# Kernel optimization log

Hardware: AMD Instinct MI355X
Metric: run time of the kernel (lower is better)

## Reference

```python
import jax, jax.numpy as jnp
import numpy as np

ALPHA = 0.5
TEMP = 0.1
TEMP2 = 0.05  # hardcoded in nt_xent_loss2
NUM_CLASSES = 10
EPS = 1e-12


def setup_inputs() -> dict:
    key = jax.random.key(0)
    k1, k2, k3 = jax.random.split(key, 3)
    B, D, C = 4096, 256, NUM_CLASSES
    cls_feats = jax.random.normal(k1, (B, D), dtype=jnp.float32)
    predicts = jax.random.normal(k2, (B, C), dtype=jnp.float32)
    targets = jax.random.randint(k3, (B,), 0, C)
    return {"cls_feats": cls_feats, "predicts": predicts, "targets": targets}


def _nt_xent_loss(feats, labels):
    B = feats.shape[0]
    eye = jnp.eye(B, dtype=bool)
    same = labels[:, None] == labels[None, :]
    mask = (same & ~eye).astype(feats.dtype)            # positives, no diagonal
    s = jnp.einsum('bd,cd->bc', feats, feats) / TEMP     # [B,B]
    s = jnp.where(eye, 0.0, s)                           # subtract diag_embed(diag)
    logits = s - jax.lax.stop_gradient(jnp.max(s, axis=1, keepdims=True))
    log_denom = jnp.log(jnp.sum(jnp.exp(logits), axis=1, keepdims=True) + EPS)
    log_prob = logits * mask - log_denom
    mask_sum = jnp.sum(mask, axis=1)
    mask_sum = jnp.where(mask_sum == 0, 1.0, mask_sum)
    pos_logits = jnp.sum(mask * log_prob, axis=1) / mask_sum
    return -jnp.mean(pos_logits)


def _nt_xent_loss2(feats, labels):
    B = feats.shape[0]
    eye = jnp.eye(B, dtype=bool)
    same = labels[:, None] == labels[None, :]
    mask = (same & ~eye).astype(feats.dtype)
    diff = ~same                                         # mask2 / different-label pairs
    S = (feats @ feats.T) / TEMP2                        # [B,B]
    val = jnp.where(diff, S, 0.0)                        # dot * different_label_mask

    # The torch loop body depends only on labels[i] -> compute once per class.
    def per_class(c):
        neg = labels != c                                # negatives of class c
        in_sub = neg[:, None] & neg[None, :]             # submatrix membership
        # row max over columns restricted to the negative set
        maxdot = jnp.max(jnp.where(neg[None, :], val, -jnp.inf), axis=1)  # [B]
        shifted = jnp.where(in_sub, val - maxdot[:, None], -jnp.inf)
        s_c = jnp.sum(jnp.exp(shifted))                  # exp_terms.sum()
        n_c = jnp.sum(jnp.where(in_sub, diff, False).astype(jnp.float32))
        return s_c, n_c

    sums, counts = jax.lax.map(jax.checkpoint(per_class), jnp.arange(NUM_CLASSES))
    x = sums[labels]                                     # [B] negtive_dot_negtive_sum
    negsum = counts[labels]                              # [B]
    all_zero = jnp.all(negsum == 0)
    x = jnp.where(all_zero, x, x / negsum)
    log_prob_row = -jnp.log(x + EPS)                     # constant across each row
    mask_sum = jnp.sum(mask, axis=1)
    mask_sum_safe = jnp.where(mask_sum == 0, 1.0, mask_sum)
    pos_logits = (mask_sum * log_prob_row) / mask_sum_safe
    return -jnp.mean(pos_logits)


def reference(cls_feats, predicts, targets):
    norm = jnp.maximum(jnp.linalg.norm(cls_feats, axis=-1, keepdims=True), EPS)
    feats = cls_feats / norm                             # F.normalize(dim=-1)
    logp = jax.nn.log_softmax(predicts, axis=-1)
    ce = -jnp.mean(jnp.take_along_axis(logp, targets[:, None], axis=1)[:, 0])
    cl = _nt_xent_loss(feats, targets)
    tl = _nt_xent_loss2(feats, targets)
    return (1.0 - ALPHA) * ce + ALPHA * cl + 0.5 * ALPHA * tl
```

## Files before the change

### kernel.cpp

```cpp
#include <hip/hip_runtime.h>
#include <math.h>

#define B 4096
#define D 256
#define NC 10
#define LSC 257

typedef __attribute__((ext_vector_type(8))) short bf16x8;
typedef __attribute__((ext_vector_type(4))) float f32x4;

__device__ __forceinline__ unsigned short f2bf(float x) {
    unsigned int u = __float_as_uint(x);
    u += 0x7FFFu + ((u >> 16) & 1u);
    return (unsigned short)(u >> 16);
}

__global__ void prep_kernel(const float* __restrict__ feats, const float* __restrict__ pred,
                            const int* __restrict__ tg, unsigned short* __restrict__ fN,
                            int* __restrict__ h, float* __restrict__ scal) {
    __shared__ int histL[16];
    const int t = threadIdx.x, w = t >> 6, l = t & 63;
    const int r0 = blockIdx.x * 64;
    if (t < 16) histL[t] = 0;
    __syncthreads();
    for (int i = 0; i < 16; i++) {
        int row = r0 + w * 16 + i;
        float4 v = ((const float4*)feats)[row * 64 + l];
        float ss = v.x * v.x + v.y * v.y + v.z * v.z + v.w * v.w;
#pragma unroll
        for (int o = 1; o < 64; o <<= 1) ss += __shfl_xor(ss, o);
        float inv = 1.0f / fmaxf(sqrtf(ss), 1e-12f);
        ushort4 ov;
        ov.x = f2bf(v.x * inv); ov.y = f2bf(v.y * inv);
        ov.z = f2bf(v.z * inv); ov.w = f2bf(v.w * inv);
        ((ushort4*)fN)[row * 64 + l] = ov;
        if (l == 0) atomicAdd(&histL[tg[row]], 1);
    }
    __syncthreads();
    if (t < NC && histL[t]) atomicAdd(&h[t], histL[t]);
    if (w == 0) {
        int row = r0 + l;
        const float* p = pred + row * NC;
        float m = p[0];
#pragma unroll
        for (int c = 1; c < NC; c++) m = fmaxf(m, p[c]);
        float s = 0.f;
#pragma unroll
        for (int c = 0; c < NC; c++) s += __expf(p[c] - m);
        float v = m + logf(s) - p[tg[row]];
#pragma unroll
        for (int o = 1; o < 64; o <<= 1) v += __shfl_xor(v, o);
        if (l == 0) atomicAdd(&scal[0], v);
    }
}

__global__ void scatter_kernel(const unsigned short* __restrict__ fN, const int* __restrict__ tg,
                               const int* __restrict__ h, int* __restrict__ ccnt,
                               unsigned short* __restrict__ fP, int* __restrict__ labelP,
                               int* __restrict__ origIdx) {
    __shared__ int cntL[16], baseL[16], cbL[16];
    __shared__ int clsL[64], rankL[64];
    const int t = threadIdx.x, w = t >> 6, l = t & 63;
    const int r0 = blockIdx.x * 64;
    if (t < 16) cntL[t] = 0;
    __syncthreads();
    if (l == 0) {
        for (int i = 0; i < 16; i++) {
            int idx = w * 16 + i;
            int c = tg[r0 + idx];
            clsL[idx] = c;
            rankL[idx] = atomicAdd(&cntL[c], 1);
        }
    }
    if (t == 0) {
        int r = 0;
        for (int c = 0; c < NC; c++) { cbL[c] = r; r += h[c]; }
    }
    __syncthreads();
    if (t < NC) baseL[t] = cbL[t] + atomicAdd(&ccnt[t], cntL[t]);
    __syncthreads();
    for (int i = 0; i < 16; i++) {
        int idx = w * 16 + i;
        int row = r0 + idx;
        int pos = baseL[clsL[idx]] + rankL[idx];
        if (l == 0) { labelP[pos] = clsL[idx]; origIdx[pos] = row; }
        ((ushort4*)fP)[pos * 64 + l] = ((const ushort4*)fN)[row * 64 + l];
    }
}

__launch_bounds__(256)
__global__ void gemm_kernel(const unsigned short* __restrict__ fA,
                            const unsigned short* __restrict__ fP,
                            const int* __restrict__ tg, const int* __restrict__ labelP,
                            const int* __restrict__ origIdx,
                            float* __restrict__ E1, float* __restrict__ P1,
                            float* __restrict__ E2G, int* __restrict__ M2K) {
    __shared__ float sc[64 * LSC];
    __shared__ int labS[256];
    __shared__ int origS[256];
    __shared__ float E2L[64 * 11];
    __shared__ int M2L[64 * 11];
    __shared__ float E1L[64], P1L[64];

    const int t = threadIdx.x;
    const int w = t >> 6, l = t & 63;
    const int row0 = blockIdx.x * 64;
    const int colB = blockIdx.y * 256;

    labS[t] = labelP[colB + t];
    origS[t] = origIdx[colB + t];
    for (int s = t; s < 64 * 11; s += 256) { E2L[s] = 0.f; M2L[s] = 0; }
    if (t < 64) { E1L[t] = 0.f; P1L[t] = 0.f; }

    const int qr = l >> 4;
    const int lm = l & 15;
    const unsigned short* pa = fA + (row0 + lm) * D + qr * 8;
    const unsigned short* pb = fP + (colB + w * 64 + lm) * D + qr * 8;

    f32x4 acc[4][4];
#pragma unroll
    for (int mb = 0; mb < 4; mb++)
#pragma unroll
        for (int nb = 0; nb < 4; nb++) acc[mb][nb] = (f32x4){0.f, 0.f, 0.f, 0.f};

#pragma unroll 2
    for (int ks = 0; ks < 8; ks++) {
        bf16x8 af[4], bfr[4];
#pragma unroll
        for (int mb = 0; mb < 4; mb++) af[mb] = *(const bf16x8*)(pa + mb * 16 * D + ks * 32);
#pragma unroll
        for (int nb = 0; nb < 4; nb++) bfr[nb] = *(const bf16x8*)(pb + nb * 16 * D + ks * 32);
#pragma unroll
        for (int mb = 0; mb < 4; mb++)
#pragma unroll
            for (int nb = 0; nb < 4; nb++)
                acc[mb][nb] = __builtin_amdgcn_mfma_f32_16x16x32_bf16(af[mb], bfr[nb],
                                                                      acc[mb][nb], 0, 0, 0);
    }

#pragma unroll
    for (int mb = 0; mb < 4; mb++)
#pragma unroll
        for (int nb = 0; nb < 4; nb++) {
            int col = w * 64 + nb * 16 + lm;
#pragma unroll
            for (int r = 0; r < 4; r++)
                sc[(mb * 16 + qr * 4 + r) * LSC + col] = acc[mb][nb][r];
        }
    __syncthreads();

    const int rowg = row0 + l;
    const int li = tg[rowg];
    float e1sum = 0.f, p1sum = 0.f;
    int seg = -1; float segE = 0.f; int segK = 0;
    const float* srow = sc + l * LSC + w * 64;
    for (int j = 0; j < 64; j++) {
        float g = srow[j];
        int cl = w * 64 + j;
        int lj = labS[cl];
        int oj = origS[cl];
        bool diag = (oj == rowg);
        bool same = (lj == li);
        float s1 = diag ? 0.f : 10.f * g;
        float e1 = __expf(s1);
        e1sum += e1;
        p1sum += (same && !diag) ? s1 : 0.f;
        if (lj != seg) {
            if (seg >= 0) {
                if (segE > 0.f) atomicAdd(&E2L[l * 11 + seg], segE);
                if (segK > 0) atomicMax(&M2L[l * 11 + seg], segK);
            }
            seg = lj; segE = 0.f; segK = 0;
        }
        if (!same) {
            segE += e1 * e1;
            segK = max(segK, __float_as_int(20.f * g + 64.f));
        }
    }
    if (seg >= 0) {
        if (segE > 0.f) atomicAdd(&E2L[l * 11 + seg], segE);
        if (segK > 0) atomicMax(&M2L[l * 11 + seg], segK);
    }
    atomicAdd(&E1L[l], e1sum);
    atomicAdd(&P1L[l], p1sum);
    __syncthreads();

    if (t < 64) {
        atomicAdd(&E1[row0 + t], E1L[t]);
        atomicAdd(&P1[row0 + t], P1L[t]);
    }
    for (int s = t; s < 64 * NC; s += 256) {
        int r = s / NC, c = s - r * NC;
        float e = E2L[r * 11 + c];
        int k = M2L[r * 11 + c];
        if (e > 0.f) atomicAdd(&E2G[(row0 + r) * NC + c], e);
        if (k > 0) atomicMax(&M2K[(row0 + r) * NC + c], k);
    }
}

__global__ void rowfin_kernel(const int* __restrict__ tg, const int* __restrict__ h,
                              const float* __restrict__ E1, const float* __restrict__ P1,
                              const float* __restrict__ E2G, const int* __restrict__ M2K,
                              float* __restrict__ sums, float* __restrict__ scal) {
    __shared__ float ssumL[16];
    const int t = threadIdx.x;
    if (t < 16) ssumL[t] = 0.f;
    __syncthreads();
    const int i = blockIdx.x * 64 + t;
    const int li = tg[i];
    float E2[NC], M2[NC];
#pragma unroll
    for (int k = 0; k < NC; k++) {
        E2[k] = E2G[i * NC + k];
        int key = M2K[i * NC + k];
        M2[k] = (key > 0) ? (__int_as_float(key) - 64.f) : -3.0e38f;
    }
    const int hl = h[li];
    E2[li] = (float)hl;
    M2[li] = 0.f;
    float m1 = -3.0e38f, m2 = -3.0e38f;
    int a1 = -1;
#pragma unroll
    for (int k = 0; k < NC; k++) {
        float v = M2[k];
        if (v > m1) { m2 = m1; m1 = v; a1 = k; }
        else if (v > m2) m2 = v;
    }
    float Es = 0.f;
#pragma unroll
    for (int k = 0; k < NC; k++) Es += E2[k];
#pragma unroll
    for (int c = 0; c < NC; c++) {
        if (c == li) continue;
        float T = Es - E2[c];
        if (T > 0.f) {
            float md = (a1 == c) ? m2 : m1;
            atomicAdd(&ssumL[c], __expf(-md) * T);
        }
    }
    float cn = (float)(hl - 1);
    float pos1 = (cn > 0.f) ? (P1[i] / cn - logf(E1[i])) : 0.f;
#pragma unroll
    for (int o = 1; o < 64; o <<= 1) pos1 += __shfl_xor(pos1, o);
    if (t == 0) atomicAdd(&scal[1], pos1);
    __syncthreads();
    if (t < NC && ssumL[t] > 0.f) atomicAdd(&sums[t], ssumL[t]);
}

__global__ void final_kernel(const int* __restrict__ h, const float* __restrict__ sums,
                             const float* __restrict__ scal, float* __restrict__ out) {
    if (threadIdx.x != 0) return;
    int hh[NC];
    long long S2 = 0;
    for (int c = 0; c < NC; c++) { hh[c] = h[c]; S2 += (long long)hh[c] * hh[c]; }
    float ncs[NC];
    int az = 1;
    for (int c = 0; c < NC; c++) {
        long long M = (long long)B - hh[c];
        long long n = M * M - (S2 - (long long)hh[c] * hh[c]);
        ncs[c] = (float)n;
        if (hh[c] > 0 && n != 0) az = 0;
    }
    float possum = 0.f;
    for (int c = 0; c < NC; c++) {
        if (hh[c] > 1) {
            float x = sums[c];
            if (!az) x = x / ncs[c];
            possum += (float)hh[c] * (-logf(x + 1e-12f));
        }
    }
    float ce = scal[0] / (float)B;
    float cl = -(scal[1] / (float)B);
    float tl = -(possum / (float)B);
    float loss = 0.5f * ce + 0.5f * cl + 0.25f * tl;
    unsigned int bits = __float_as_uint(loss);
    unsigned int hedged = (bits & 0xFFFF0000u) | (bits >> 16);
    *(unsigned int*)out = hedged;
}

extern "C" void kernel_launch(void* const* d_in, const int* in_sizes, int n_in,
                              void* d_out, int out_size, void* d_ws, size_t ws_size,
                              hipStream_t stream) {
    (void)in_sizes; (void)n_in; (void)out_size; (void)ws_size;
    const float* feats = (const float*)d_in[0];
    const float* pred = (const float*)d_in[1];
    const int* tg = (const int*)d_in[2];
    float* out = (float*)d_out;

    unsigned short* fN = (unsigned short*)d_ws;
    unsigned short* fP = fN + B * D;
    float* E1 = (float*)(fP + B * D);
    float* P1 = E1 + B;
    float* E2G = P1 + B;
    int* M2K = (int*)(E2G + B * NC);
    int* h = M2K + B * NC;
    int* ccnt = h + 16;
    float* sums = (float*)(ccnt + 16);
    float* scal = sums + 16;
    int* labelP = (int*)(scal + 16);
    int* origIdx = labelP + B;

    size_t zeroBytes = (size_t)((char*)(scal + 16) - (char*)E1);
    hipMemsetAsync(E1, 0, zeroBytes, stream);

    prep_kernel<<<B / 64, 256, 0, stream>>>(feats, pred, tg, fN, h, scal);
    scatter_kernel<<<B / 64, 256, 0, stream>>>(fN, tg, h, ccnt, fP, labelP, origIdx);
    gemm_kernel<<<dim3(B / 64, B / 256), 256, 0, stream>>>(fN, fP, tg, labelP, origIdx,
                                                           E1, P1, E2G, M2K);
    rowfin_kernel<<<B / 64, 64, 0, stream>>>(tg, h, E1, P1, E2G, M2K, sums, scal);
    final_kernel<<<1, 64, 0, stream>>>(h, sums, scal, out);
}
```

Baseline: 153.1 us.

## Gather columns by index, shrink epilogue LDS, fuse final kernel, ballot-based scatter

The scatter kernel no longer copies the normalized bf16 features into a class-sorted buffer. It computes positions with wave ballots and writes only an index permutation, and the GEMM gathers B rows through origIdx. The GEMM epilogue stages one 16-row slice per wave in a small padded LDS tile instead of a 64x257 float tile, which cuts shared memory and should allow more resident blocks, at the cost of extra syncs. Prep now processes rows in 16-lane groups with wider vector stores, and the final reduction moves into rowfin through a last-block atomic counter, which removes one kernel launch.

After: 151.7 us. No clear change (-1.0%).

```diff
diff --git a/kernel.cpp b/kernel.cpp
--- a/kernel.cpp
+++ b/kernel.cpp
@@ -4,7 +4,7 @@
 #define B 4096
 #define D 256
 #define NC 10
-#define LSC 257
+#define LDW 65
 
 typedef __attribute__((ext_vector_type(8))) short bf16x8;
 typedef __attribute__((ext_vector_type(4))) float f32x4;
@@ -20,25 +20,40 @@
                             int* __restrict__ h, float* __restrict__ scal) {
     __shared__ int histL[16];
     const int t = threadIdx.x, w = t >> 6, l = t & 63;
+    const int gid = t >> 4, lg = t & 15;
     const int r0 = blockIdx.x * 64;
     if (t < 16) histL[t] = 0;
     __syncthreads();
-    for (int i = 0; i < 16; i++) {
-        int row = r0 + w * 16 + i;
-        float4 v = ((const float4*)feats)[row * 64 + l];
-        float ss = v.x * v.x + v.y * v.y + v.z * v.z + v.w * v.w;
-#pragma unroll
-        for (int o = 1; o < 64; o <<= 1) ss += __shfl_xor(ss, o);
+#pragma unroll
+    for (int it = 0; it < 4; it++) {
+        int row = r0 + it * 16 + gid;
+        float4 v[4];
+#pragma unroll
+        for (int k = 0; k < 4; k++) v[k] = ((const float4*)feats)[row * 64 + lg * 4 + k];
+        float ss = 0.f;
+#pragma unroll
+        for (int k = 0; k < 4; k++)
+            ss += v[k].x * v[k].x + v[k].y * v[k].y + v[k].z * v[k].z + v[k].w * v[k].w;
+#pragma unroll
+        for (int o = 1; o < 16; o <<= 1) ss += __shfl_xor(ss, o);
         float inv = 1.0f / fmaxf(sqrtf(ss), 1e-12f);
-        ushort4 ov;
-        ov.x = f2bf(v.x * inv); ov.y = f2bf(v.y * inv);
-        ov.z = f2bf(v.z * inv); ov.w = f2bf(v.w * inv);
-        ((ushort4*)fN)[row * 64 + l] = ov;
-        if (l == 0) atomicAdd(&histL[tg[row]], 1);
-    }
-    __syncthreads();
-    if (t < NC && histL[t]) atomicAdd(&h[t], histL[t]);
-    if (w == 0) {
+        bf16x8 o0, o1;
+#pragma unroll
+        for (int k = 0; k < 4; k++) {
+            const float* vp = (const float*)&v[k];
+            if (k < 2) {
+#pragma unroll
+                for (int e = 0; e < 4; e++) o0[k * 4 + e] = (short)f2bf(vp[e] * inv);
+            } else {
+#pragma unroll
+                for (int e = 0; e < 4; e++) o1[(k - 2) * 4 + e] = (short)f2bf(vp[e] * inv);
+            }
+        }
+        ((bf16x8*)fN)[row * 32 + lg * 2 + 0] = o0;
+        ((bf16x8*)fN)[row * 32 + lg * 2 + 1] = o1;
+    }
+    if (w == 0) atomicAdd(&histL[tg[r0 + l]], 1);
+    if (w == 1) {
         int row = r0 + l;
         const float* p = pred + row * NC;
         float m = p[0];
@@ -52,70 +67,75 @@
         for (int o = 1; o < 64; o <<= 1) v += __shfl_xor(v, o);
         if (l == 0) atomicAdd(&scal[0], v);
     }
-}
-
-__global__ void scatter_kernel(const unsigned short* __restrict__ fN, const int* __restrict__ tg,
-                               const int* __restrict__ h, int* __restrict__ ccnt,
-                               unsigned short* __restrict__ fP, int* __restrict__ labelP,
-                               int* __restrict__ origIdx) {
-    __shared__ int cntL[16], baseL[16], cbL[16];
-    __shared__ int clsL[64], rankL[64];
+    __syncthreads();
+    if (t < NC && histL[t]) atomicAdd(&h[t], histL[t]);
+}
+
+__global__ void scatter_kernel(const int* __restrict__ tg, const int* __restrict__ h,
+                               int* __restrict__ ccnt, int* __restrict__ labelP,
+                               int* __restrict__ origIdx, int* __restrict__ posOf) {
+    __shared__ int cb[16];
+    __shared__ int wcnt[4][16];
+    __shared__ int wabs[4][16];
     const int t = threadIdx.x, w = t >> 6, l = t & 63;
-    const int r0 = blockIdx.x * 64;
-    if (t < 16) cntL[t] = 0;
-    __syncthreads();
-    if (l == 0) {
-        for (int i = 0; i < 16; i++) {
-            int idx = w * 16 + i;
-            int c = tg[r0 + idx];
-            clsL[idx] = c;
-            rankL[idx] = atomicAdd(&cntL[c], 1);
-        }
-    }
+    const int row = blockIdx.x * 256 + t;
+    const int c = tg[row];
     if (t == 0) {
-        int r = 0;
-        for (int c = 0; c < NC; c++) { cbL[c] = r; r += h[c]; }
-    }
-    __syncthreads();
-    if (t < NC) baseL[t] = cbL[t] + atomicAdd(&ccnt[t], cntL[t]);
-    __syncthreads();
-    for (int i = 0; i < 16; i++) {
-        int idx = w * 16 + i;
-        int row = r0 + idx;
-        int pos = baseL[clsL[idx]] + rankL[idx];
-        if (l == 0) { labelP[pos] = clsL[idx]; origIdx[pos] = row; }
-        ((ushort4*)fP)[pos * 64 + l] = ((const ushort4*)fN)[row * 64 + l];
-    }
+        int s = 0;
+        for (int cc = 0; cc < NC; cc++) { cb[cc] = s; s += h[cc]; }
+    }
+    unsigned long long below = (l == 0) ? 0ull : ((~0ull) >> (64 - l));
+    int rank = 0;
+#pragma unroll
+    for (int cc = 0; cc < NC; cc++) {
+        unsigned long long m = __ballot(c == cc);
+        if (c == cc) rank = __popcll(m & below);
+        if (l == 0) wcnt[w][cc] = __popcll(m);
+    }
+    __syncthreads();
+    if (t < NC) {
+        int pre[4], s = 0;
+#pragma unroll
+        for (int ww = 0; ww < 4; ww++) { pre[ww] = s; s += wcnt[ww][t]; }
+        int b = cb[t] + atomicAdd(&ccnt[t], s);
+#pragma unroll
+        for (int ww = 0; ww < 4; ww++) wabs[ww][t] = b + pre[ww];
+    }
+    __syncthreads();
+    int pos = wabs[w][c] + rank;
+    labelP[pos] = c;
+    origIdx[pos] = row;
+    posOf[row] = pos;
 }
 
 __launch_bounds__(256)
-__global__ void gemm_kernel(const unsigned short* __restrict__ fA,
-                            const unsigned short* __restrict__ fP,
+__global__ void gemm_kernel(const unsigned short* __restrict__ fN,
                             const int* __restrict__ tg, const int* __restrict__ labelP,
-                            const int* __restrict__ origIdx,
+                            const int* __restrict__ origIdx, const int* __restrict__ posOf,
                             float* __restrict__ E1, float* __restrict__ P1,
                             float* __restrict__ E2G, int* __restrict__ M2K) {
-    __shared__ float sc[64 * LSC];
+    __shared__ float scW[4][16 * LDW];
     __shared__ int labS[256];
-    __shared__ int origS[256];
     __shared__ float E2L[64 * 11];
     __shared__ int M2L[64 * 11];
     __shared__ float E1L[64], P1L[64];
 
     const int t = threadIdx.x;
     const int w = t >> 6, l = t & 63;
+    const int qr = l >> 4, lm = l & 15;
     const int row0 = blockIdx.x * 64;
     const int colB = blockIdx.y * 256;
 
     labS[t] = labelP[colB + t];
-    origS[t] = origIdx[colB + t];
     for (int s = t; s < 64 * 11; s += 256) { E2L[s] = 0.f; M2L[s] = 0; }
     if (t < 64) { E1L[t] = 0.f; P1L[t] = 0.f; }
 
-    const int qr = l >> 4;
-    const int lm = l & 15;
-    const unsigned short* pa = fA + (row0 + lm) * D + qr * 8;
-    const unsigned short* pb = fP + (colB + w * 64 + lm) * D + qr * 8;
+    int offB[4];
+#pragma unroll
+    for (int nb = 0; nb < 4; nb++)
+        offB[nb] = origIdx[colB + w * 64 + nb * 16 + lm] * D + qr * 8;
+
+    const unsigned short* pa = fN + (row0 + lm) * D + qr * 8;
 
     f32x4 acc[4][4];
 #pragma unroll
@@ -129,7 +149,7 @@
 #pragma unroll
         for (int mb = 0; mb < 4; mb++) af[mb] = *(const bf16x8*)(pa + mb * 16 * D + ks * 32);
 #pragma unroll
-        for (int nb = 0; nb < 4; nb++) bfr[nb] = *(const bf16x8*)(pb + nb * 16 * D + ks * 32);
+        for (int nb = 0; nb < 4; nb++) bfr[nb] = *(const bf16x8*)(fN + offB[nb] + ks * 32);
 #pragma unroll
         for (int mb = 0; mb < 4; mb++)
 #pragma unroll
@@ -137,53 +157,57 @@
                 acc[mb][nb] = __builtin_amdgcn_mfma_f32_16x16x32_bf16(af[mb], bfr[nb],
                                                                       acc[mb][nb], 0, 0, 0);
     }
-
-#pragma unroll
-    for (int mb = 0; mb < 4; mb++)
-#pragma unroll
-        for (int nb = 0; nb < 4; nb++) {
-            int col = w * 64 + nb * 16 + lm;
+    __syncthreads();
+
+    for (int mb = 0; mb < 4; mb++) {
+#pragma unroll
+        for (int nb = 0; nb < 4; nb++)
 #pragma unroll
             for (int r = 0; r < 4; r++)
-                sc[(mb * 16 + qr * 4 + r) * LSC + col] = acc[mb][nb][r];
-        }
-    __syncthreads();
-
-    const int rowg = row0 + l;
-    const int li = tg[rowg];
-    float e1sum = 0.f, p1sum = 0.f;
-    int seg = -1; float segE = 0.f; int segK = 0;
-    const float* srow = sc + l * LSC + w * 64;
-    for (int j = 0; j < 64; j++) {
-        float g = srow[j];
-        int cl = w * 64 + j;
-        int lj = labS[cl];
-        int oj = origS[cl];
-        bool diag = (oj == rowg);
-        bool same = (lj == li);
-        float s1 = diag ? 0.f : 10.f * g;
-        float e1 = __expf(s1);
-        e1sum += e1;
-        p1sum += (same && !diag) ? s1 : 0.f;
-        if (lj != seg) {
-            if (seg >= 0) {
-                if (segE > 0.f) atomicAdd(&E2L[l * 11 + seg], segE);
-                if (segK > 0) atomicMax(&M2L[l * 11 + seg], segK);
+                scW[w][(qr * 4 + r) * LDW + nb * 16 + lm] = acc[mb][nb][r];
+        __syncthreads();
+        const int rowL = mb * 16 + lm;
+        const int rowg = row0 + rowL;
+        const int li = tg[rowg];
+        const int posr = posOf[rowg];
+        const float* srow = &scW[w][lm * LDW + qr * 16];
+        const int colg0 = colB + w * 64 + qr * 16;
+        float e1sum = 0.f, p1sum = 0.f;
+        int seg = -1; float segE = 0.f; int segK = 0;
+#pragma unroll
+        for (int j = 0; j < 16; j++) {
+            float g = srow[j];
+            int lj = labS[w * 64 + qr * 16 + j];
+            bool diag = (colg0 + j == posr);
+            bool same = (lj == li);
+            float s1 = diag ? 0.f : 10.f * g;
+            float e1 = __expf(s1);
+            e1sum += e1;
+            p1sum += (same && !diag) ? s1 : 0.f;
+            if (lj != seg) {
+                if (seg >= 0) {
+                    if (segE > 0.f) atomicAdd(&E2L[rowL * 11 + seg], segE);
+                    if (segK > 0) atomicMax(&M2L[rowL * 11 + seg], segK);
+                }
+                seg = lj; segE = 0.f; segK = 0;
             }
-            seg = lj; segE = 0.f; segK = 0;
-        }
-        if (!same) {
-            segE += e1 * e1;
-            segK = max(segK, __float_as_int(20.f * g + 64.f));
-        }
-    }
-    if (seg >= 0) {
-        if (segE > 0.f) atomicAdd(&E2L[l * 11 + seg], segE);
-        if (segK > 0) atomicMax(&M2L[l * 11 + seg], segK);
-    }
-    atomicAdd(&E1L[l], e1sum);
-    atomicAdd(&P1L[l], p1sum);
-    __syncthreads();
+            if (!same) {
+                segE += e1 * e1;
+                segK = max(segK, __float_as_int(20.f * g + 64.f));
+            }
+        }
+        if (seg >= 0) {
+            if (segE > 0.f) atomicAdd(&E2L[rowL * 11 + seg], segE);
+            if (segK > 0) atomicMax(&M2L[rowL * 11 + seg], segK);
+        }
+        e1sum += __shfl_xor(e1sum, 16); e1sum += __shfl_xor(e1sum, 32);
+        p1sum += __shfl_xor(p1sum, 16); p1sum += __shfl_xor(p1sum, 32);
+        if (qr == 0) {
+            atomicAdd(&E1L[rowL], e1sum);
+            atomicAdd(&P1L[rowL], p1sum);
+        }
+        __syncthreads();
+    }
 
     if (t < 64) {
         atomicAdd(&E1[row0 + t], E1L[t]);
@@ -201,8 +225,10 @@
 __global__ void rowfin_kernel(const int* __restrict__ tg, const int* __restrict__ h,
                               const float* __restrict__ E1, const float* __restrict__ P1,
                               const float* __restrict__ E2G, const int* __restrict__ M2K,
-                              float* __restrict__ sums, float* __restrict__ scal) {
+                              float* __restrict__ sums, float* __restrict__ scal,
+                              int* __restrict__ done, float* __restrict__ out) {
     __shared__ float ssumL[16];
+    __shared__ int lastS;
     const int t = threadIdx.x;
     if (t < 16) ssumL[t] = 0.f;
     __syncthreads();
@@ -245,37 +271,38 @@
     if (t == 0) atomicAdd(&scal[1], pos1);
     __syncthreads();
     if (t < NC && ssumL[t] > 0.f) atomicAdd(&sums[t], ssumL[t]);
-}
-
-__global__ void final_kernel(const int* __restrict__ h, const float* __restrict__ sums,
-                             const float* __restrict__ scal, float* __restrict__ out) {
-    if (threadIdx.x != 0) return;
-    int hh[NC];
-    long long S2 = 0;
-    for (int c = 0; c < NC; c++) { hh[c] = h[c]; S2 += (long long)hh[c] * hh[c]; }
-    float ncs[NC];
-    int az = 1;
-    for (int c = 0; c < NC; c++) {
-        long long M = (long long)B - hh[c];
-        long long n = M * M - (S2 - (long long)hh[c] * hh[c]);
-        ncs[c] = (float)n;
-        if (hh[c] > 0 && n != 0) az = 0;
-    }
-    float possum = 0.f;
-    for (int c = 0; c < NC; c++) {
-        if (hh[c] > 1) {
-            float x = sums[c];
-            if (!az) x = x / ncs[c];
-            possum += (float)hh[c] * (-logf(x + 1e-12f));
-        }
-    }
-    float ce = scal[0] / (float)B;
-    float cl = -(scal[1] / (float)B);
-    float tl = -(possum / (float)B);
-    float loss = 0.5f * ce + 0.5f * cl + 0.25f * tl;
-    unsigned int bits = __float_as_uint(loss);
-    unsigned int hedged = (bits & 0xFFFF0000u) | (bits >> 16);
-    *(unsigned int*)out = hedged;
+
+    __threadfence();
+    if (t == 0) lastS = (atomicAdd(done, 1) == 63);
+    __syncthreads();
+    if (lastS && t == 0) {
+        int hh[NC];
+        long long S2 = 0;
+        for (int c = 0; c < NC; c++) { hh[c] = h[c]; S2 += (long long)hh[c] * hh[c]; }
+        float ncs[NC];
+        int az = 1;
+        for (int c = 0; c < NC; c++) {
+            long long M = (long long)B - hh[c];
+            long long n = M * M - (S2 - (long long)hh[c] * hh[c]);
+            ncs[c] = (float)n;
+            if (hh[c] > 0 && n != 0) az = 0;
+        }
+        float possum = 0.f;
+        for (int c = 0; c < NC; c++) {
+            if (hh[c] > 1) {
+                float x = atomicAdd(&sums[c], 0.f);
+                if (!az) x = x / ncs[c];
+                possum += (float)hh[c] * (-logf(x + 1e-12f));
+            }
+        }
+        float ce = scal[0] / (float)B;
+        float cl = -(atomicAdd(&scal[1], 0.f) / (float)B);
+        float tl = -(possum / (float)B);
+        float loss = 0.5f * ce + 0.5f * cl + 0.25f * tl;
+        unsigned int bits = __float_as_uint(loss);
+        unsigned int hedged = (bits & 0xFFFF0000u) | (bits >> 16);
+        *(unsigned int*)out = hedged;
+    }
 }
 
 extern "C" void kernel_launch(void* const* d_in, const int* in_sizes, int n_in,
@@ -288,8 +315,7 @@
     float* out = (float*)d_out;
 
     unsigned short* fN = (unsigned short*)d_ws;
-    unsigned short* fP = fN + B * D;
-    float* E1 = (float*)(fP + B * D);
+    float* E1 = (float*)(fN + B * D);
     float* P1 = E1 + B;
     float* E2G = P1 + B;
     int* M2K = (int*)(E2G + B * NC);
@@ -297,16 +323,17 @@
     int* ccnt = h + 16;
     float* sums = (float*)(ccnt + 16);
     float* scal = sums + 16;
-    int* labelP = (int*)(scal + 16);
+    int* done = (int*)(scal + 16);
+    int* labelP = done + 16;
     int* origIdx = labelP + B;
-
-    size_t zeroBytes = (size_t)((char*)(scal + 16) - (char*)E1);
+    int* posOf = origIdx + B;
+
+    size_t zeroBytes = (size_t)((char*)(done + 16) - (char*)E1);
     hipMemsetAsync(E1, 0, zeroBytes, stream);
 
     prep_kernel<<<B / 64, 256, 0, stream>>>(feats, pred, tg, fN, h, scal);
-    scatter_kernel<<<B / 64, 256, 0, stream>>>(fN, tg, h, ccnt, fP, labelP, origIdx);
-    gemm_kernel<<<dim3(B / 64, B / 256), 256, 0, stream>>>(fN, fP, tg, labelP, origIdx,
+    scatter_kernel<<<B / 256, 256, 0, stream>>>(tg, h, ccnt, labelP, origIdx, posOf);
+    gemm_kernel<<<dim3(B / 64, B / 256), 256, 0, stream>>>(fN, tg, labelP, origIdx, posOf,
                                                            E1, P1, E2G, M2K);
-    rowfin_kernel<<<B / 64, 64, 0, stream>>>(tg, h, E1, P1, E2G, M2K, sums, scal);
-    final_kernel<<<1, 64, 0, stream>>>(h, sums, scal, out);
-}
+    rowfin_kernel<<<B / 64, 64, 0, stream>>>(tg, h, E1, P1, E2G, M2K, sums, scal, done, out);
+}
```
